# Kernel tuning notes

Hardware: AMD Instinct MI355X
Metric: run time of the kernel (lower is better)

Reference implementation:

```python
import jax, jax.numpy as jnp
import numpy as np

B, S, D, H, L, OUT = 4, 1024, 1024, 16, 6, 512
HD = D // H
EPS = 1e-5


def _positional_encoding(seq, dim):
    pos = np.arange(seq, dtype=np.float32)[:, None]          # [S,1]
    i = np.arange(0, dim, 2, dtype=np.float32)[None, :]       # even indices
    div = np.power(10000.0, 2.0 * i / dim)                    # repo's (nonstandard) exponent
    pe = np.zeros((seq, dim), dtype=np.float32)
    pe[:, 0::2] = np.sin(pos / div)
    pe[:, 1::2] = np.cos(pos / div)
    return jnp.asarray(pe)[None]                               # [1,S,D]


def _causal_mask(seq):
    r = jnp.arange(seq)
    m = jnp.where(r[None, :] > r[:, None], jnp.float32(-jnp.inf), jnp.float32(0.0))
    return m[None, None]                                       # [1,1,S,S]


def setup_inputs() -> dict:
    key = jax.random.key(0)
    ks = jax.random.split(key, 10)
    sc = 0.02
    inp = {
        'x':      jax.random.normal(ks[0], (B, S, D), jnp.float32),
        'pe':     _positional_encoding(S, D),
        'mask':   _causal_mask(S),
        'ln1_g':  jnp.ones((L, D), jnp.float32),
        'ln1_b':  jnp.zeros((L, D), jnp.float32),
        'wq':     jax.random.normal(ks[1], (L, D, D), jnp.float32) * sc,
        'wk':     jax.random.normal(ks[2], (L, D, D), jnp.float32) * sc,
        'wv':     jax.random.normal(ks[3], (L, D, D), jnp.float32) * sc,
        'wo':     jax.random.normal(ks[4], (L, D, D), jnp.float32) * sc,
        'ln2_g':  jnp.ones((L, D), jnp.float32),
        'ln2_b':  jnp.zeros((L, D), jnp.float32),
        'wf':     jax.random.normal(ks[5], (L, D, D), jnp.float32) * sc,
        'lnf_g':  jnp.ones((D,), jnp.float32),
        'lnf_b':  jnp.zeros((D,), jnp.float32),
        'w_out':  jax.random.normal(ks[6], (OUT, D), jnp.float32) * sc,
    }
    return inp


def _layer_norm(x, g, b):
    mu = jnp.mean(x, axis=-1, keepdims=True)
    var = jnp.mean(jnp.square(x - mu), axis=-1, keepdims=True)
    return (x - mu) * jax.lax.rsqrt(var + EPS) * g + b


def _split_heads(x):
    b, s, d = x.shape
    return x.reshape(b, s, H, HD).transpose(0, 2, 1, 3)  # [B,H,S,HD]


def reference(x, pe, mask, ln1_g, ln1_b, wq, wk, wv, wo, ln2_g, ln2_b, wf, lnf_g, lnf_b, w_out):
    h = x + pe
    scale = 1.0 / jnp.sqrt(jnp.float32(HD))
    for l in range(wq.shape[0]):
        h_ = _layer_norm(h, ln1_g[l], ln1_b[l])
        q = _split_heads(jnp.einsum('bsd,ed->bse', h_, wq[l]))
        k = _split_heads(jnp.einsum('bsd,ed->bse', h_, wk[l]))
        v = _split_heads(jnp.einsum('bsd,ed->bse', h_, wv[l]))
        scores = jnp.einsum('bhqd,bhkd->bhqk', q, k) * scale + mask  # [B,H,S,S]
        probs = jax.nn.softmax(scores, axis=-1)
        attn = jnp.einsum('bhqk,bhkd->bhqd', probs, v)
        attn = attn.transpose(0, 2, 1, 3).reshape(h.shape)            # combine heads
        h = h + jnp.einsum('bsd,ed->bse', attn, wo[l])
        h_ = _layer_norm(h, ln2_g[l], ln2_b[l])
        h = h + jnp.einsum('bsd,ed->bse', h_, wf[l])                  # FFN = plain linear (no activation, as in source)
    h = _layer_norm(h, lnf_g, lnf_b)
    return jnp.einsum('bsd,od->bso', h, w_out)
```

## Files before the change

kernel.cpp:

```cpp
#include <hip/hip_runtime.h>
#include <hip/hip_bf16.h>
#include <stdint.h>

#define BATCH 4
#define SEQ   1024
#define DIM   1024
#define NH    16
#define HDIM  64
#define NLAYER 6
#define NOUT  512
#define NTOK  (BATCH*SEQ)
#define LOG2E 1.44269504088896f
#define NEG_BIG (-1e30f)
#define VTS   72

using bf16 = __hip_bfloat16;
typedef __attribute__((ext_vector_type(4))) float f32x4;
typedef __attribute__((ext_vector_type(8))) short bf16x8;

typedef __attribute__((address_space(1))) void as1_void;
typedef __attribute__((address_space(3))) void as3_void;

__device__ __forceinline__ float bf2f(short u) {
  union { unsigned int i; float f; } c;
  c.i = ((unsigned int)(unsigned short)u) << 16;
  return c.f;
}

__device__ __forceinline__ short f2bs(float f) {
  bf16 h = __float2bfloat16(f);
  return *(short*)&h;
}

__device__ __forceinline__ float exp_clamped(float x) {
  return exp2f(fmaxf(x, -100.f) * LOG2E);
}

__device__ __forceinline__ float loadf(const void* p, size_t i, bool f32) {
  return f32 ? ((const float*)p)[i] : __bfloat162float(((const bf16*)p)[i]);
}

__device__ __forceinline__ void g2l16(const void* g, void* l) {
  __builtin_amdgcn_global_load_lds((const as1_void*)g, (as3_void*)l, 16, 0, 0);
}

__global__ void sniff(const unsigned int* __restrict__ w, int* __restrict__ flag) {
  const int lane = threadIdx.x;
  const unsigned int word = w[lane];
  const int e2 = (word >> 7) & 0xFF;
  const bool bf16ish = (e2 >= 0x60) && (e2 <= 0x8F);
  const unsigned long long m = __ballot(bf16ish);
  if (lane == 0) *flag = (__popcll(m) >= 48) ? 0 : 1;
}

__global__ __launch_bounds__(256) void convert_w(const void* __restrict__ src,
                                                 bf16* __restrict__ dst,
                                                 const int* __restrict__ flag) {
  const size_t i = ((size_t)blockIdx.x * 256 + threadIdx.x) * 8;
  if (*flag) {
    const float* s = (const float*)src + i;
#pragma unroll
    for (int e = 0; e < 8; ++e) dst[i + e] = __float2bfloat16(s[e]);
  } else {
    *(bf16x8*)(dst + i) = *(const bf16x8*)((const bf16*)src + i);
  }
}

template<int EPI>
__device__ __forceinline__ void gemm_body(const bf16* __restrict__ A,
                                          const bf16* __restrict__ W,
                                          void* __restrict__ C,
                                          const int* __restrict__ flag,
                                          int N, int m0, int n0) {
  __shared__ __align__(16) bf16 lA[128 * 32];
  __shared__ __align__(16) bf16 lB[128 * 32];
  const int tid  = threadIdx.x;
  const int wave = tid >> 6;
  const int lane = tid & 63;
  const int quad = lane >> 4;
  const int l16  = lane & 15;
  const int wm = (wave >> 1) * 64;
  const int wn = (wave & 1) * 64;
  const int K = DIM;

  const int r0 = tid >> 2;
  const int c0 = (tid & 3) * 8;
  const int r1 = (tid + 256) >> 2;

  bool f32out = false;
  if (EPI == 2) f32out = (*flag != 0);

  f32x4 acc[4][4];
#pragma unroll
  for (int i = 0; i < 4; ++i)
#pragma unroll
    for (int j = 0; j < 4; ++j) acc[i][j] = (f32x4){0.f, 0.f, 0.f, 0.f};

  for (int k0 = 0; k0 < K; k0 += 32) {
    __syncthreads();
    g2l16(A + (size_t)(m0 + r0) * K + k0 + c0, lA + 512 * wave);
    g2l16(A + (size_t)(m0 + r1) * K + k0 + c0, lA + 2048 + 512 * wave);
    g2l16(W + (size_t)(n0 + r0) * K + k0 + c0, lB + 512 * wave);
    g2l16(W + (size_t)(n0 + r1) * K + k0 + c0, lB + 2048 + 512 * wave);
    __builtin_amdgcn_s_waitcnt(0);
    __syncthreads();

    bf16x8 af[4], bfr[4];
#pragma unroll
    for (int i = 0; i < 4; ++i) {
      af[i]  = *(const bf16x8*)(lA + (wm + i * 16 + l16) * 32 + quad * 8);
      bfr[i] = *(const bf16x8*)(lB + (wn + i * 16 + l16) * 32 + quad * 8);
    }
#pragma unroll
    for (int i = 0; i < 4; ++i)
#pragma unroll
      for (int j = 0; j < 4; ++j)
        acc[i][j] = __builtin_amdgcn_mfma_f32_16x16x32_bf16(af[i], bfr[j], acc[i][j], 0, 0, 0);
  }

#pragma unroll
  for (int i = 0; i < 4; ++i) {
    const int rowb = m0 + wm + i * 16 + quad * 4;
#pragma unroll
    for (int j = 0; j < 4; ++j) {
      const int col = n0 + wn + j * 16 + l16;
#pragma unroll
      for (int r = 0; r < 4; ++r) {
        const size_t idx = (size_t)(rowb + r) * N + col;
        const float v = acc[i][j][r];
        if (EPI == 0) ((bf16*)C)[idx] = __float2bfloat16(v);
        else { if (f32out) ((float*)C)[idx] = v; else ((bf16*)C)[idx] = __float2bfloat16(v); }
      }
    }
  }
}

__device__ __forceinline__ void gemm64_body(const bf16* __restrict__ A,
                                            const bf16* __restrict__ W,
                                            float* __restrict__ C,
                                            int N, int m0, int n0) {
  __shared__ __align__(16) bf16 lA[64 * 32];
  __shared__ __align__(16) bf16 lB[128 * 32];
  const int tid  = threadIdx.x;
  const int wave = tid >> 6;
  const int lane = tid & 63;
  const int quad = lane >> 4;
  const int l16  = lane & 15;
  const int wm = (wave >> 1) * 32;
  const int wn = (wave & 1) * 64;
  const int K = DIM;

  const int r0 = tid >> 2;
  const int c0 = (tid & 3) * 8;
  const int r1 = (tid + 256) >> 2;

  f32x4 acc[2][4];
#pragma unroll
  for (int i = 0; i < 2; ++i)
#pragma unroll
    for (int j = 0; j < 4; ++j) acc[i][j] = (f32x4){0.f, 0.f, 0.f, 0.f};

  for (int k0 = 0; k0 < K; k0 += 32) {
    __syncthreads();
    g2l16(A + (size_t)(m0 + r0) * K + k0 + c0, lA + 512 * wave);
    g2l16(W + (size_t)(n0 + r0) * K + k0 + c0, lB + 512 * wave);
    g2l16(W + (size_t)(n0 + r1) * K + k0 + c0, lB + 2048 + 512 * wave);
    __builtin_amdgcn_s_waitcnt(0);
    __syncthreads();

    bf16x8 af[2], bfr[4];
#pragma unroll
    for (int i = 0; i < 2; ++i)
      af[i]  = *(const bf16x8*)(lA + (wm + i * 16 + l16) * 32 + quad * 8);
#pragma unroll
    for (int j = 0; j < 4; ++j)
      bfr[j] = *(const bf16x8*)(lB + (wn + j * 16 + l16) * 32 + quad * 8);
#pragma unroll
    for (int i = 0; i < 2; ++i)
#pragma unroll
      for (int j = 0; j < 4; ++j)
        acc[i][j] = __builtin_amdgcn_mfma_f32_16x16x32_bf16(af[i], bfr[j], acc[i][j], 0, 0, 0);
  }

#pragma unroll
  for (int i = 0; i < 2; ++i) {
    const int rowb = m0 + wm + i * 16 + quad * 4;
#pragma unroll
    for (int j = 0; j < 4; ++j) {
      const int col = n0 + wn + j * 16 + l16;
#pragma unroll
      for (int r = 0; r < 4; ++r)
        C[(size_t)(rowb + r) * N + col] += acc[i][j][r];
    }
  }
}

__global__ __launch_bounds__(256) void gemm_out(const bf16* __restrict__ A,
                                                const bf16* __restrict__ W,
                                                void* __restrict__ C,
                                                const int* __restrict__ flag) {
  gemm_body<2>(A, W, C, flag, NOUT, blockIdx.y * 128, blockIdx.x * 128);
}

__global__ __launch_bounds__(256) void gemm_add(const bf16* __restrict__ A,
                                                const bf16* __restrict__ W,
                                                float* __restrict__ C) {
  gemm64_body(A, W, C, DIM, blockIdx.y * 64, blockIdx.x * 128);
}

__device__ __forceinline__ bf16x8 rd_frag(const short* slab, int row, int quad) {
  const int g  = row >> 1;
  const int cc = (((row & 1) << 2) | quad) ^ (g & 7);
  return *(const bf16x8*)(slab + g * 64 + cc * 8);
}

__global__ __launch_bounds__(512, 2) void gemm_qkv_8p(const bf16* __restrict__ A,
                                                      const bf16* __restrict__ wq,
                                                      const bf16* __restrict__ wk,
                                                      const bf16* __restrict__ wv,
                                                      bf16* __restrict__ q,
                                                      bf16* __restrict__ k,
                                                      bf16* __restrict__ v) {
  __shared__ __align__(16) short lA[4 * 8192];
  __shared__ __align__(16) short lB[4 * 8192];

  const int bid = blockIdx.x;
  const int mt  = bid / 12;
  const int rm  = bid - mt * 12;
  const int sel = rm >> 2;
  const int n0  = (rm & 3) * 256;
  const int m0  = mt * 256;
  const bf16* W = (sel == 0) ? wq : (sel == 1 ? wk : wv);
  bf16* C       = (sel == 0) ? q  : (sel == 1 ? k  : v);

  const int tid  = threadIdx.x;
  const int wave = tid >> 6;
  const int lane = tid & 63;
  const int quad = lane >> 4;
  const int l16  = lane & 15;
  const int wr   = wave >> 2;
  const int wc   = wave & 3;

  const int c3   = (lane & 7) ^ (lane >> 3);
  const int sq   = c3 & 3;
  const int rsub = ((lane >> 3) << 1) | (c3 >> 2);
  const size_t aOff0 = (size_t)(m0 + wave * 32 + rsub) * DIM + sq * 8;
  const size_t aOff1 = aOff0 + (size_t)16 * DIM;
  const size_t bOff0 = (size_t)(n0 + wave * 32 + rsub) * DIM + sq * 8;
  const size_t bOff1 = bOff0 + (size_t)16 * DIM;
  const int ldsW = wave * 1024;

#define STAGE_A8(J) { short* s_ = lA + ((J) & 3) * 8192 + ldsW;                 \
    g2l16(A + aOff0 + (J) * 32, s_); g2l16(A + aOff1 + (J) * 32, s_ + 512); }
#define STAGE_B8(J) { short* s_ = lB + ((J) & 3) * 8192 + ldsW;                 \
    g2l16(W + bOff0 + (J) * 32, s_); g2l16(W + bOff1 + (J) * 32, s_ + 512); }

  f32x4 acc[8][4];
#pragma unroll
  for (int i = 0; i < 8; ++i)
#pragma unroll
    for (int jn = 0; jn < 4; ++jn) acc[i][jn] = (f32x4){0.f, 0.f, 0.f, 0.f};

  STAGE_A8(0); STAGE_B8(0);
  STAGE_A8(1); STAGE_B8(1);
  STAGE_A8(2); STAGE_B8(2);
  STAGE_B8(3);
  asm volatile("s_waitcnt vmcnt(6)" ::: "memory");
  __builtin_amdgcn_s_barrier();
  __builtin_amdgcn_sched_barrier(0);

  const int arow = wr * 128 + l16;
  const int brow = wc * 64 + l16;

  for (int jo = 0; jo < 32; jo += 4) {
#pragma unroll
    for (int ji = 0; ji < 4; ++ji) {
      const int j = jo + ji;
      const short* sA = lA + ji * 8192;
      const short* sB = lB + ji * 8192;
      bf16x8 af[4], bfv[4];
#pragma unroll
      for (int mi = 0; mi < 4; ++mi) af[mi]  = rd_frag(sA, arow + mi * 16, quad);
#pragma unroll
      for (int nj = 0; nj < 4; ++nj) bfv[nj] = rd_frag(sB, brow + nj * 16, quad);
      if (j < 29) STAGE_A8(j + 3);
      __builtin_amdgcn_s_barrier();
      asm volatile("s_waitcnt lgkmcnt(0)" ::: "memory");
      __builtin_amdgcn_sched_barrier(0);
      __builtin_amdgcn_s_setprio(1);
#pragma unroll
      for (int mi = 0; mi < 4; ++mi)
#pragma unroll
        for (int nj = 0; nj < 4; ++nj)
          acc[mi][nj] = __builtin_amdgcn_mfma_f32_16x16x32_bf16(af[mi], bfv[nj], acc[mi][nj], 0, 0, 0);
      __builtin_amdgcn_s_setprio(0);
      __builtin_amdgcn_s_barrier();
      __builtin_amdgcn_sched_barrier(0);
#pragma unroll
      for (int mi = 0; mi < 4; ++mi) af[mi] = rd_frag(sA, arow + 64 + mi * 16, quad);
      if (j < 28) STAGE_B8(j + 4);
      __builtin_amdgcn_s_barrier();
      asm volatile("s_waitcnt lgkmcnt(0)" ::: "memory");
      __builtin_amdgcn_sched_barrier(0);
      __builtin_amdgcn_s_setprio(1);
#pragma unroll
      for (int mi = 0; mi < 4; ++mi)
#pragma unroll
        for (int nj = 0; nj < 4; ++nj)
          acc[4 + mi][nj] = __builtin_amdgcn_mfma_f32_16x16x32_bf16(af[mi], bfv[nj], acc[4 + mi][nj], 0, 0, 0);
      __builtin_amdgcn_s_setprio(0);
      if (ji & 1) {
        if (j < 28) { asm volatile("s_waitcnt vmcnt(6)" ::: "memory"); }
        else        { asm volatile("s_waitcnt vmcnt(0)" ::: "memory"); }
      }
      __builtin_amdgcn_s_barrier();
      __builtin_amdgcn_sched_barrier(0);
    }
  }
#undef STAGE_A8
#undef STAGE_B8

#pragma unroll
  for (int mi = 0; mi < 8; ++mi) {
    const int rowb = m0 + wr * 128 + mi * 16 + quad * 4;
#pragma unroll
    for (int nj = 0; nj < 4; ++nj) {
      const int col = n0 + wc * 64 + nj * 16 + l16;
#pragma unroll
      for (int rr = 0; rr < 4; ++rr)
        C[(size_t)(rowb + rr) * DIM + col] = __float2bfloat16(acc[mi][nj][rr]);
    }
  }
}

__global__ __launch_bounds__(256) void add_pe(const void* __restrict__ x,
                                              const void* __restrict__ pe,
                                              float* __restrict__ h,
                                              const int* __restrict__ flag) {
  const bool f32 = (*flag != 0);
  const size_t i = (size_t)blockIdx.x * 256 + threadIdx.x;
  h[i] = loadf(x, i, f32) + loadf(pe, i & (SEQ * DIM - 1), f32);
}

__global__ __launch_bounds__(256) void layernorm(const float* __restrict__ x,
                                                 const void* __restrict__ g,
                                                 const void* __restrict__ b,
                                                 int loff,
                                                 bf16* __restrict__ y,
                                                 const int* __restrict__ flag) {
  const bool f32 = (*flag != 0);
  const int row = blockIdx.x;
  const int tid = threadIdx.x;
  const int wave = tid >> 6;
  const float* xr = x + (size_t)row * DIM;
  __shared__ float red[8];

  float v[4];
  float s = 0.f;
#pragma unroll
  for (int i = 0; i < 4; ++i) { v[i] = xr[tid + 256 * i]; s += v[i]; }
#pragma unroll
  for (int off = 32; off >= 1; off >>= 1) s += __shfl_xor(s, off);
  if ((tid & 63) == 0) red[wave] = s;
  __syncthreads();
  const float mu = (red[0] + red[1] + red[2] + red[3]) * (1.f / DIM);

  float vs = 0.f;
#pragma unroll
  for (int i = 0; i < 4; ++i) { const float d = v[i] - mu; vs += d * d; }
#pragma unroll
  for (int off = 32; off >= 1; off >>= 1) vs += __shfl_xor(vs, off);
  if ((tid & 63) == 0) red[4 + wave] = vs;
  __syncthreads();
  const float var = (red[4] + red[5] + red[6] + red[7]) * (1.f / DIM);
  const float rs = rsqrtf(var + 1e-5f);

#pragma unroll
  for (int i = 0; i < 4; ++i) {
    const int d = tid + 256 * i;
    const float gv = loadf(g, (size_t)loff + d, f32);
    const float bv = loadf(b, (size_t)loff + d, f32);
    y[(size_t)row * DIM + d] = __float2bfloat16((v[i] - mu) * rs * gv + bv);
  }
}

__global__ __launch_bounds__(256, 2) void attn_flash(const bf16* __restrict__ q,
                                                     const bf16* __restrict__ k,
                                                     const bf16* __restrict__ v,
                                                     bf16* __restrict__ o) {
  __shared__ __align__(16) short lK[64 * 64];
  __shared__ __align__(16) short lVT[64 * VTS];
  __shared__ __align__(16) short lP[4 * 16 * VTS];

  const int idx = blockIdx.x;
  const int qt = (SEQ / 64 - 1) - (idx >> 6);
  const int bh = idx & 63;
  const int hh = bh & (NH - 1);
  const int bb = bh >> 4;
  const int q0 = qt * 64;

  const int tid = threadIdx.x;
  const int wave = tid >> 6;
  const int lane = tid & 63;
  const int quad = lane >> 4;
  const int l16 = lane & 15;

  const size_t base = (size_t)bb * SEQ * DIM + hh * HDIM;
  const int qlo = q0 + wave * 16;

  bf16x8 qf[2];
  {
    const bf16* qr = q + base + (size_t)(qlo + l16) * DIM;
#pragma unroll
    for (int kc = 0; kc < 2; ++kc) {
      bf16x8 t = *(const bf16x8*)(qr + kc * 32 + quad * 8);
      bf16x8 sq;
#pragma unroll
      for (int e = 0; e < 8; ++e) sq[e] = f2bs(bf2f(t[e]) * 0.125f);
      qf[kc] = sq;
    }
  }

  float l_acc[4] = {0.f, 0.f, 0.f, 0.f};
  f32x4 oacc[4];
#pragma unroll
  for (int nb = 0; nb < 4; ++nb) oacc[nb] = (f32x4){0.f, 0.f, 0.f, 0.f};

  short* lPw = lP + wave * 16 * VTS;
  const int nt = qt + 1;

  for (int t = 0; t < nt; ++t) {
    const int kbase = t * 64;
    __syncthreads();

    {
      const int r8 = lane >> 3;
      const int cc = (lane & 7) ^ r8;
#pragma unroll
      for (int c = 0; c < 2; ++c) {
        const int row = wave * 16 + c * 8 + r8;
        g2l16(k + base + (size_t)(kbase + row) * DIM + cc * 8,
              lK + (wave * 16 + c * 8) * 64);
      }
    }

    bf16x8 vch[2];
#pragma unroll
    for (int c2 = 0; c2 < 2; ++c2) {
      const int cid = tid + c2 * 256;
      const int kk = cid >> 3;
      const int d0 = (cid & 7) * 8;
      vch[c2] = *(const bf16x8*)(v + base + (size_t)(kbase + kk) * DIM + d0);
    }
#pragma unroll
    for (int c2 = 0; c2 < 2; ++c2) {
      const int cid = tid + c2 * 256;
      const int kk = cid >> 3;
      const int d0 = (cid & 7) * 8;
#pragma unroll
      for (int e = 0; e < 8; ++e) {
        const int d = d0 + e;
        const int kks = kk ^ (((d >> 3) & 7) << 3);
        lVT[d * VTS + kks] = vch[c2][e];
      }
    }
    __builtin_amdgcn_s_waitcnt(0);
    __syncthreads();

    f32x4 s[4];
#pragma unroll
    for (int nb = 0; nb < 4; ++nb) {
      f32x4 acc = (f32x4){0.f, 0.f, 0.f, 0.f};
      const int n = nb * 16 + l16;
#pragma unroll
      for (int kc = 0; kc < 2; ++kc) {
        const int cidx = (kc * 4 + quad) ^ (n & 7);
        bf16x8 kf = *(const bf16x8*)(lK + n * 64 + cidx * 8);
        acc = __builtin_amdgcn_mfma_f32_16x16x32_bf16(qf[kc], kf, acc, 0, 0, 0);
      }
      s[nb] = acc;
    }

    if (kbase + 63 > qlo) {
#pragma unroll
      for (int nb = 0; nb < 4; ++nb) {
        const int j = kbase + nb * 16 + l16;
#pragma unroll
        for (int r = 0; r < 4; ++r)
          if (j > qlo + quad * 4 + r) s[nb][r] = NEG_BIG;
      }
    }

#pragma unroll
    for (int nb = 0; nb < 4; ++nb) {
#pragma unroll
      for (int r = 0; r < 4; ++r) {
        const float p = exp_clamped(s[nb][r]);
        l_acc[r] += p;
        lPw[(quad * 4 + r) * VTS + nb * 16 + l16] = f2bs(p);
      }
    }

    __builtin_amdgcn_s_waitcnt(0);
    bf16x8 pf[2];
#pragma unroll
    for (int kc = 0; kc < 2; ++kc)
      pf[kc] = *(const bf16x8*)(lPw + l16 * VTS + kc * 32 + quad * 8);

#pragma unroll
    for (int nb = 0; nb < 4; ++nb) {
      const int n = nb * 16 + l16;
      const int swz = ((n >> 3) & 7) << 3;
#pragma unroll
      for (int kc = 0; kc < 2; ++kc) {
        const int kchunk = (kc * 32 + quad * 8) ^ swz;
        bf16x8 vf = *(const bf16x8*)(lVT + n * VTS + kchunk);
        oacc[nb] = __builtin_amdgcn_mfma_f32_16x16x32_bf16(pf[kc], vf, oacc[nb], 0, 0, 0);
      }
    }
  }

  float linv[4];
#pragma unroll
  for (int r = 0; r < 4; ++r) {
    float ts = l_acc[r];
#pragma unroll
    for (int off = 8; off >= 1; off >>= 1) ts += __shfl_xor(ts, off);
    linv[r] = 1.f / ts;
  }
#pragma unroll
  for (int nb = 0; nb < 4; ++nb)
#pragma unroll
    for (int r = 0; r < 4; ++r) {
      const int qrow = q0 + wave * 16 + quad * 4 + r;
      o[base + (size_t)qrow * DIM + nb * 16 + l16] =
          __float2bfloat16(oacc[nb][r] * linv[r]);
    }
}

extern "C" void kernel_launch(void* const* d_in, const int* in_sizes, int n_in,
                              void* d_out, int out_size, void* d_ws, size_t ws_size,
                              hipStream_t stream) {
  const void* x    = d_in[0];
  const void* pe   = d_in[1];
  const void* ln1g = d_in[3];
  const void* ln1b = d_in[4];
  const void* wq   = d_in[5];
  const void* wk   = d_in[6];
  const void* wv   = d_in[7];
  const void* wo   = d_in[8];
  const void* ln2g = d_in[9];
  const void* ln2b = d_in[10];
  const void* wf   = d_in[11];
  const void* lnfg = d_in[12];
  const void* lnfb = d_in[13];
  const void* wout = d_in[14];

  const size_t MB = 1u << 20;
  char* ws = (char*)d_ws;
  int*  flag = (int*)ws;
  bf16* wqc  = (bf16*)(ws + 1 * MB);
  bf16* wkc  = (bf16*)(ws + 13 * MB);
  bf16* wvc  = (bf16*)(ws + 25 * MB);
  bf16* woc  = (bf16*)(ws + 37 * MB);
  bf16* wfc  = (bf16*)(ws + 49 * MB);
  bf16* woutc= (bf16*)(ws + 61 * MB);
  float* h   = (float*)(ws + 62 * MB);
  bf16* hn   = (bf16*)(ws + 78 * MB);
  bf16* qb   = (bf16*)(ws + 86 * MB);
  bf16* kb   = (bf16*)(ws + 94 * MB);
  bf16* vb   = (bf16*)(ws + 102 * MB);
  bf16* ab   = hn;

  sniff<<<1, 64, 0, stream>>>((const unsigned int*)wq, flag);

  const int WBLK = (NLAYER * DIM * DIM) / (256 * 8);
  convert_w<<<WBLK, 256, 0, stream>>>(wq, wqc, flag);
  convert_w<<<WBLK, 256, 0, stream>>>(wk, wkc, flag);
  convert_w<<<WBLK, 256, 0, stream>>>(wv, wvc, flag);
  convert_w<<<WBLK, 256, 0, stream>>>(wo, woc, flag);
  convert_w<<<WBLK, 256, 0, stream>>>(wf, wfc, flag);
  convert_w<<<(NOUT * DIM) / (256 * 8), 256, 0, stream>>>(wout, woutc, flag);

  add_pe<<<NTOK * DIM / 256, 256, 0, stream>>>(x, pe, h, flag);

  for (int l = 0; l < NLAYER; ++l) {
    const size_t woff = (size_t)l << 20;
    const int poff = l * DIM;
    layernorm<<<NTOK, 256, 0, stream>>>(h, ln1g, ln1b, poff, hn, flag);
    gemm_qkv_8p<<<dim3(192), 512, 0, stream>>>(hn, wqc + woff, wkc + woff, wvc + woff,
                                               qb, kb, vb);
    attn_flash<<<dim3(BATCH * NH * (SEQ / 64)), 256, 0, stream>>>(qb, kb, vb, ab);
    gemm_add<<<dim3(8, 64), 256, 0, stream>>>(ab, woc + woff, h);
    layernorm<<<NTOK, 256, 0, stream>>>(h, ln2g, ln2b, poff, hn, flag);
    gemm_add<<<dim3(8, 64), 256, 0, stream>>>(hn, wfc + woff, h);
  }

  layernorm<<<NTOK, 256, 0, stream>>>(h, lnfg, lnfb, 0, hn, flag);
  gemm_out<<<dim3(4, 32), 256, 0, stream>>>(hn, woutc, d_out, flag);
}
```

Before: 982.7 us.

## Replace residual GEMMs with pipelined 8-wave kernel and merge weight conversions

The simple residual-add GEMM, which synchronised fully on every K step, is replaced by a 512-thread kernel. It uses 256x64 tiles, a 4-stage LDS ring loaded through global_load_lds, swizzled fragment reads, interleaved barriers with s_setprio, and partial vmcnt waits so loads overlap MFMA work. This attacks the latency-bound loop in the output-projection and FFN GEMMs, which run twice per layer. Separately, the six weight-conversion launches are merged into one kernel to cut launch overhead. The new tiling launches 256 blocks with a narrow N tile, which trades B-operand reuse for parallelism and adds complex, fragile synchronisation.

```diff
diff --git a/kernel.cpp b/kernel.cpp
--- a/kernel.cpp
+++ b/kernel.cpp
@@ -53,10 +53,22 @@
   if (lane == 0) *flag = (__popcll(m) >= 48) ? 0 : 1;
 }
 
-__global__ __launch_bounds__(256) void convert_w(const void* __restrict__ src,
-                                                 bf16* __restrict__ dst,
-                                                 const int* __restrict__ flag) {
-  const size_t i = ((size_t)blockIdx.x * 256 + threadIdx.x) * 8;
+__global__ __launch_bounds__(256) void convert_all(
+    const void* __restrict__ s0, const void* __restrict__ s1,
+    const void* __restrict__ s2, const void* __restrict__ s3,
+    const void* __restrict__ s4, const void* __restrict__ s5,
+    bf16* __restrict__ d0, bf16* __restrict__ d1, bf16* __restrict__ d2,
+    bf16* __restrict__ d3, bf16* __restrict__ d4, bf16* __restrict__ d5,
+    const int* __restrict__ flag) {
+  int b = blockIdx.x;
+  const void* src; bf16* dst;
+  if      (b <  3072) { src = s0; dst = d0; }
+  else if (b <  6144) { src = s1; dst = d1; b -= 3072; }
+  else if (b <  9216) { src = s2; dst = d2; b -= 6144; }
+  else if (b < 12288) { src = s3; dst = d3; b -= 9216; }
+  else if (b < 15360) { src = s4; dst = d4; b -= 12288; }
+  else                { src = s5; dst = d5; b -= 15360; }
+  const size_t i = ((size_t)b * 256 + threadIdx.x) * 8;
   if (*flag) {
     const float* s = (const float*)src + i;
 #pragma unroll
@@ -135,77 +147,11 @@
   }
 }
 
-__device__ __forceinline__ void gemm64_body(const bf16* __restrict__ A,
-                                            const bf16* __restrict__ W,
-                                            float* __restrict__ C,
-                                            int N, int m0, int n0) {
-  __shared__ __align__(16) bf16 lA[64 * 32];
-  __shared__ __align__(16) bf16 lB[128 * 32];
-  const int tid  = threadIdx.x;
-  const int wave = tid >> 6;
-  const int lane = tid & 63;
-  const int quad = lane >> 4;
-  const int l16  = lane & 15;
-  const int wm = (wave >> 1) * 32;
-  const int wn = (wave & 1) * 64;
-  const int K = DIM;
-
-  const int r0 = tid >> 2;
-  const int c0 = (tid & 3) * 8;
-  const int r1 = (tid + 256) >> 2;
-
-  f32x4 acc[2][4];
-#pragma unroll
-  for (int i = 0; i < 2; ++i)
-#pragma unroll
-    for (int j = 0; j < 4; ++j) acc[i][j] = (f32x4){0.f, 0.f, 0.f, 0.f};
-
-  for (int k0 = 0; k0 < K; k0 += 32) {
-    __syncthreads();
-    g2l16(A + (size_t)(m0 + r0) * K + k0 + c0, lA + 512 * wave);
-    g2l16(W + (size_t)(n0 + r0) * K + k0 + c0, lB + 512 * wave);
-    g2l16(W + (size_t)(n0 + r1) * K + k0 + c0, lB + 2048 + 512 * wave);
-    __builtin_amdgcn_s_waitcnt(0);
-    __syncthreads();
-
-    bf16x8 af[2], bfr[4];
-#pragma unroll
-    for (int i = 0; i < 2; ++i)
-      af[i]  = *(const bf16x8*)(lA + (wm + i * 16 + l16) * 32 + quad * 8);
-#pragma unroll
-    for (int j = 0; j < 4; ++j)
-      bfr[j] = *(const bf16x8*)(lB + (wn + j * 16 + l16) * 32 + quad * 8);
-#pragma unroll
-    for (int i = 0; i < 2; ++i)
-#pragma unroll
-      for (int j = 0; j < 4; ++j)
-        acc[i][j] = __builtin_amdgcn_mfma_f32_16x16x32_bf16(af[i], bfr[j], acc[i][j], 0, 0, 0);
-  }
-
-#pragma unroll
-  for (int i = 0; i < 2; ++i) {
-    const int rowb = m0 + wm + i * 16 + quad * 4;
-#pragma unroll
-    for (int j = 0; j < 4; ++j) {
-      const int col = n0 + wn + j * 16 + l16;
-#pragma unroll
-      for (int r = 0; r < 4; ++r)
-        C[(size_t)(rowb + r) * N + col] += acc[i][j][r];
-    }
-  }
-}
-
 __global__ __launch_bounds__(256) void gemm_out(const bf16* __restrict__ A,
                                                 const bf16* __restrict__ W,
                                                 void* __restrict__ C,
                                                 const int* __restrict__ flag) {
   gemm_body<2>(A, W, C, flag, NOUT, blockIdx.y * 128, blockIdx.x * 128);
-}
-
-__global__ __launch_bounds__(256) void gemm_add(const bf16* __restrict__ A,
-                                                const bf16* __restrict__ W,
-                                                float* __restrict__ C) {
-  gemm64_body(A, W, C, DIM, blockIdx.y * 64, blockIdx.x * 128);
 }
 
 __device__ __forceinline__ bf16x8 rd_frag(const short* slab, int row, int quad) {
@@ -329,6 +275,119 @@
 #pragma unroll
       for (int rr = 0; rr < 4; ++rr)
         C[(size_t)(rowb + rr) * DIM + col] = __float2bfloat16(acc[mi][nj][rr]);
+    }
+  }
+}
+
+__global__ __launch_bounds__(512, 2) void gemm_add_8p(const bf16* __restrict__ A,
+                                                      const bf16* __restrict__ W,
+                                                      float* __restrict__ C) {
+  __shared__ __align__(16) short lA[4 * 8192];
+  __shared__ __align__(16) short lB[4 * 2048];
+
+  const int bid = blockIdx.x;
+  const int m0 = (bid >> 4) * 256;
+  const int n0 = (bid & 15) * 64;
+
+  const int tid  = threadIdx.x;
+  const int wave = tid >> 6;
+  const int lane = tid & 63;
+  const int quad = lane >> 4;
+  const int l16  = lane & 15;
+  const int wr   = wave >> 1;
+  const int wc   = wave & 1;
+
+  const int c3   = (lane & 7) ^ (lane >> 3);
+  const int sq   = c3 & 3;
+  const int rsub = ((lane >> 3) << 1) | (c3 >> 2);
+  const size_t aOff0 = (size_t)(m0 + wave * 32 + rsub) * DIM + sq * 8;
+  const size_t aOff1 = aOff0 + (size_t)16 * DIM;
+  const size_t bOff  = (size_t)(n0 + wave * 16 + rsub) * DIM + sq * 8;
+  const int ldsWA = wave * 1024;
+  const int ldsWB = wave * 512;
+
+#define SA8(J) { short* s_ = lA + ((J) & 3) * 8192 + ldsWA;                     \
+    g2l16(A + aOff0 + (J) * 32, s_); g2l16(A + aOff1 + (J) * 32, s_ + 512); }
+#define SB8(J) if (wave < 4) { short* s_ = lB + ((J) & 3) * 2048 + ldsWB;       \
+    g2l16(W + bOff + (J) * 32, s_); }
+
+  f32x4 acc[4][2];
+#pragma unroll
+  for (int i = 0; i < 4; ++i)
+#pragma unroll
+    for (int jn = 0; jn < 2; ++jn) acc[i][jn] = (f32x4){0.f, 0.f, 0.f, 0.f};
+
+  SA8(0); SB8(0);
+  SA8(1); SB8(1);
+  SA8(2); SB8(2);
+  SB8(3);
+  if (wave < 4) { asm volatile("s_waitcnt vmcnt(4)" ::: "memory"); }
+  else          { asm volatile("s_waitcnt vmcnt(2)" ::: "memory"); }
+  __builtin_amdgcn_s_barrier();
+  __builtin_amdgcn_sched_barrier(0);
+
+  const int arow = wr * 64 + l16;
+  const int brow = wc * 32 + l16;
+
+  for (int jo = 0; jo < 32; jo += 4) {
+#pragma unroll
+    for (int ji = 0; ji < 4; ++ji) {
+      const int j = jo + ji;
+      const short* sA = lA + ji * 8192;
+      const short* sB = lB + ji * 2048;
+      bf16x8 af[2], bfv[2];
+      af[0]  = rd_frag(sA, arow,      quad);
+      af[1]  = rd_frag(sA, arow + 16, quad);
+      bfv[0] = rd_frag(sB, brow,      quad);
+      bfv[1] = rd_frag(sB, brow + 16, quad);
+      if (j < 29) SA8(j + 3);
+      __builtin_amdgcn_s_barrier();
+      asm volatile("s_waitcnt lgkmcnt(0)" ::: "memory");
+      __builtin_amdgcn_sched_barrier(0);
+      __builtin_amdgcn_s_setprio(1);
+      acc[0][0] = __builtin_amdgcn_mfma_f32_16x16x32_bf16(af[0], bfv[0], acc[0][0], 0, 0, 0);
+      acc[0][1] = __builtin_amdgcn_mfma_f32_16x16x32_bf16(af[0], bfv[1], acc[0][1], 0, 0, 0);
+      acc[1][0] = __builtin_amdgcn_mfma_f32_16x16x32_bf16(af[1], bfv[0], acc[1][0], 0, 0, 0);
+      acc[1][1] = __builtin_amdgcn_mfma_f32_16x16x32_bf16(af[1], bfv[1], acc[1][1], 0, 0, 0);
+      __builtin_amdgcn_s_setprio(0);
+      __builtin_amdgcn_s_barrier();
+      __builtin_amdgcn_sched_barrier(0);
+      af[0] = rd_frag(sA, arow + 32, quad);
+      af[1] = rd_frag(sA, arow + 48, quad);
+      if (j < 28) SB8(j + 4);
+      __builtin_amdgcn_s_barrier();
+      asm volatile("s_waitcnt lgkmcnt(0)" ::: "memory");
+      __builtin_amdgcn_sched_barrier(0);
+      __builtin_amdgcn_s_setprio(1);
+      acc[2][0] = __builtin_amdgcn_mfma_f32_16x16x32_bf16(af[0], bfv[0], acc[2][0], 0, 0, 0);
+      acc[2][1] = __builtin_amdgcn_mfma_f32_16x16x32_bf16(af[0], bfv[1], acc[2][1], 0, 0, 0);
+      acc[3][0] = __builtin_amdgcn_mfma_f32_16x16x32_bf16(af[1], bfv[0], acc[3][0], 0, 0, 0);
+      acc[3][1] = __builtin_amdgcn_mfma_f32_16x16x32_bf16(af[1], bfv[1], acc[3][1], 0, 0, 0);
+      __builtin_amdgcn_s_setprio(0);
+      if (ji & 1) {
+        if (j < 28) {
+          if (wave < 4) { asm volatile("s_waitcnt vmcnt(4)" ::: "memory"); }
+          else          { asm volatile("s_waitcnt vmcnt(2)" ::: "memory"); }
+        } else {
+          asm volatile("s_waitcnt vmcnt(0)" ::: "memory");
+        }
+      }
+      __builtin_amdgcn_s_barrier();
+      __builtin_amdgcn_sched_barrier(0);
+    }
+  }
+#undef SA8
+#undef SB8
+
+#pragma unroll
+  for (int mi = 0; mi < 4; ++mi) {
+    const int rowb = m0 + wr * 64 + mi * 16 + quad * 4;
+#pragma unroll
+    for (int nj = 0; nj < 2; ++nj) {
+      const int col = n0 + wc * 32 + nj * 16 + l16;
+#pragma unroll
+      for (int rr = 0; rr < 4; ++rr)
+        C[(size_t)(rowb + rr) * DIM + col] += acc[mi][nj][rr];
     }
   }
 }
@@ -574,13 +633,8 @@
 
   sniff<<<1, 64, 0, stream>>>((const unsigned int*)wq, flag);
 
-  const int WBLK = (NLAYER * DIM * DIM) / (256 * 8);
-  convert_w<<<WBLK, 256, 0, stream>>>(wq, wqc, flag);
-  convert_w<<<WBLK, 256, 0, stream>>>(wk, wkc, flag);
-  convert_w<<<WBLK, 256, 0, stream>>>(wv, wvc, flag);
-  convert_w<<<WBLK, 256, 0, stream>>>(wo, woc, flag);
-  convert_w<<<WBLK, 256, 0, stream>>>(wf, wfc, flag);
-  convert_w<<<(NOUT * DIM) / (256 * 8), 256, 0, stream>>>(wout, woutc, flag);
+  convert_all<<<15616, 256, 0, stream>>>(wq, wk, wv, wo, wf, wout,
+                                         wqc, wkc, wvc, woc, wfc, woutc, flag);
 
   add_pe<<<NTOK * DIM / 256, 256, 0, stream>>>(x, pe, h, flag);
 
@@ -591,9 +645,9 @@
     gemm_qkv_8p<<<dim3(192), 512, 0, stream>>>(hn, wqc + woff, wkc + woff, wvc + woff,
                                                qb, kb, vb);
     attn_flash<<<dim3(BATCH * NH * (SEQ / 64)), 256, 0, stream>>>(qb, kb, vb, ab);
-    gemm_add<<<dim3(8, 64), 256, 0, stream>>>(ab, woc + woff, h);
+    gemm_add_8p<<<dim3(256), 512, 0, stream>>>(ab, woc + woff, h);
     layernorm<<<NTOK, 256, 0, stream>>>(h, ln2g, ln2b, poff, hn, flag);
-    gemm_add<<<dim3(8, 64), 256, 0, stream>>>(hn, wfc + woff, h);
+    gemm_add_8p<<<dim3(256), 512, 0, stream>>>(hn, wfc + woff, h);
   }
 
   layernorm<<<NTOK, 256, 0, stream>>>(h, lnfg, lnfb, 0, hn, flag);
```

After: 1.009 ms. 2.6% more time.
